# Optimization experiments

Hardware: AMD Instinct MI355X
Metric: run time of the kernel (lower is better)

## Reference

```python
import jax, jax.numpy as jnp
import numpy as np

H_DIM = 1024
GROUPS = [(256, 2), (128, 3), (64, 2)]  # (subspace_dim d, count n), descending d; sum(d*n)=1024
NUM_STEPS = 32
BLOCK_LEN = 4096
BZ = 256
NUM_UNITS = sum(n for _, n in GROUPS)  # 7 subspaces total
EPS_Q = 1e-8   # query norm clamp (torch clamp(min=1e-08))
EPS_K = 1e-3   # key norm clamp (torch clamp(min=0.001))
EPS_COS = 1e-8 # F.cosine_similarity eps


def _split_subspaces(h):
    """h: [bz, H] (already rotated) -> list of [n_i, bz, d_i] per group.
    Mirrors _get_subspace_h: split along features, view [bz,n,d], transpose(0,1)."""
    out, off = [], 0
    bz = h.shape[0]
    for d, n in GROUPS:
        chunk = h[:, off:off + d * n].reshape(bz, n, d).transpose(1, 0, 2)
        out.append(chunk)
        off += d * n
    return out


def setup_inputs() -> dict:
    key = jax.random.key(0)
    k1, k2, k3 = jax.random.split(key, 3)
    query = jax.random.normal(k1, (BZ, H_DIM), jnp.float32)
    keys = jax.random.normal(k2, (NUM_STEPS, BLOCK_LEN, H_DIM), jnp.float32)
    A = jax.random.normal(k3, (H_DIM, H_DIM), jnp.float32)
    R, _ = jnp.linalg.qr(A)  # orthogonal rotation weight (torch orthogonal parametrization)
    return {"query": query, "keys": keys, "R": R}


def reference(query, keys, R):
    # differentiable rotated query subspaces
    query_sub = _split_subspaces(query @ R)  # list of [n, bz, d]

    # ---- no-grad top-1 retrieval over num_steps key blocks ----
    q_sub_sg = [jax.lax.stop_gradient(q) for q in query_sub]
    q_normed = [q / jnp.clip(jnp.linalg.norm(q, axis=-1, keepdims=True), EPS_Q, None)
                for q in q_sub_sg]
    keys_sg = jax.lax.stop_gradient(keys)
    R_sg = jax.lax.stop_gradient(R)

    def step(carry, key_block):
        best_val, best_vec = carry
        k_sub = _split_subspaces(key_block @ R_sg)
        sims = []
        for q, k in zip(q_normed, k_sub):
            kn = k / jnp.clip(jnp.linalg.norm(k, axis=-1, keepdims=True), EPS_K, None)
            sims.append(jnp.einsum('nbd,nld->nbl', q, kn))
        sim = jnp.concatenate(sims, axis=0)      # [U, bz, L]
        max_v = sim.max(axis=-1)                  # [U, bz]
        max_idx = sim.argmax(axis=-1)             # [U, bz]
        cand_vec = key_block[max_idx]             # [U, bz, H] gather of raw (unrotated) keys
        m = max_v > best_val                      # masked update: most_sim_value[m]=...
        best_val = jnp.where(m, max_v, best_val)
        best_vec = jnp.where(m[..., None], cand_vec, best_vec)
        return (best_val, best_vec), None

    init = (-jnp.ones((NUM_UNITS, BZ), jnp.float32),
            jnp.zeros((NUM_UNITS, BZ, H_DIM), jnp.float32))
    (_, best_vec), _ = jax.lax.scan(step, init, keys_sg)

    # ---- differentiable loss: rotate retrieved vectors through R ----
    rotated = (best_vec.reshape(NUM_UNITS * BZ, H_DIM) @ R).reshape(NUM_UNITS, BZ, H_DIM)
    sims = []
    off_u, off_c = 0, 0
    for i, (d, n) in enumerate(GROUPS):
        chunk = rotated[off_u:off_u + n, :, off_c:off_c + n * d]   # [n, bz, n*d]
        chunk = chunk.reshape(n, BZ, n, d).transpose(0, 2, 1, 3)   # [n, n, bz, d]
        diag = chunk[jnp.arange(n), jnp.arange(n)]                 # [n, bz, d] (eye-mask select)
        q = query_sub[i]                                           # [n, bz, d]
        num = jnp.sum(q * diag, axis=-1)
        den = (jnp.clip(jnp.linalg.norm(q, axis=-1), EPS_COS, None) *
               jnp.clip(jnp.linalg.norm(diag, axis=-1), EPS_COS, None))
        cos = num / den                                            # [n, bz]
        sims.append(cos.mean(axis=1) * d)                          # weight by subspace dim
        off_u += n
        off_c += n * d
    sim_total = jnp.concatenate(sims).sum() / H_DIM
    return -sim_total
```

## Files before the change

### kernel.cpp

```cpp
#include <hip/hip_runtime.h>
#include <stdint.h>

static constexpr int Hd   = 1024;
static constexpr int BZn  = 256;
static constexpr int MTOT = 131072;
static constexpr int BM   = 64;
static constexpr int NU   = 7;

typedef float  f32x4  __attribute__((ext_vector_type(4)));
typedef short  bf16x8 __attribute__((ext_vector_type(8)));
typedef unsigned short u16;

__device__ __forceinline__ u16 f2bf(float f) {
    unsigned int u = __float_as_uint(f);
    unsigned int r = (u + 0x7FFFu + ((u >> 16) & 1u)) >> 16;
    return (u16)r;
}
__device__ __forceinline__ float bf2f(u16 h) {
    return __uint_as_float(((unsigned int)h) << 16);
}


__global__ void k_qrot(const float* __restrict__ query, const float* __restrict__ R,
                       float* __restrict__ Qrot) {
    __shared__ float qt[4][Hd];
    const int t = threadIdx.x;
    const int r0 = blockIdx.x * 4;
    for (int r = 0; r < 4; ++r)
        *(float4*)(&qt[r][t * 4]) = *(const float4*)(query + (long long)(r0 + r) * Hd + t * 4);
    __syncthreads();
    float acc[4][4] = {};
    for (int k = 0; k < Hd; ++k) {
        float4 rv = *(const float4*)(R + (long long)k * Hd + t * 4);
#pragma unroll
        for (int r = 0; r < 4; ++r) {
            float qv = qt[r][k];
            acc[r][0] += qv * rv.x; acc[r][1] += qv * rv.y;
            acc[r][2] += qv * rv.z; acc[r][3] += qv * rv.w;
        }
    }
    for (int r = 0; r < 4; ++r) {
        float4 o; o.x = acc[r][0]; o.y = acc[r][1]; o.z = acc[r][2]; o.w = acc[r][3];
        *(float4*)(Qrot + (long long)(r0 + r) * Hd + t * 4) = o;
    }
}

__global__ void k_rpack(const float* __restrict__ R, u16* __restrict__ Rpack) {
    const int gt = blockIdx.x * 256 + threadIdx.x;
    const int frag = gt >> 6, lam = gt & 63;
    const int cblk = frag >> 5, kblk = frag & 31;
    const int c  = cblk * 16 + (lam & 15);
    const int k0 = kblk * 32 + (lam >> 4) * 8;
    union { bf16x8 v; u16 u[8]; } p;
#pragma unroll
    for (int j = 0; j < 8; ++j) p.u[j] = f2bf(R[(long long)(k0 + j) * Hd + c]);
    *(bf16x8*)(Rpack + (long long)frag * 512 + lam * 8) = p.v;
}

__global__ void k_qpack(const float* __restrict__ Qrot, u16* __restrict__ Qpack) {
    const int gt = blockIdx.x * 256 + threadIdx.x;
    const int frag = gt >> 6, lam = gt & 63;
    const int cblk = frag >> 4, qblk = frag & 15;
    const int q  = qblk * 16 + (lam & 15);
    const int c0 = cblk * 32 + (lam >> 4) * 8;
    union { bf16x8 v; u16 u[8]; } p;
#pragma unroll
    for (int j = 0; j < 8; ++j) p.u[j] = f2bf(Qrot[(long long)q * Hd + c0 + j]);
    *(bf16x8*)(Qpack + (long long)frag * 512 + lam * 8) = p.v;
}

static constexpr int LDS_TOT = 163840;

__global__ __launch_bounds__(512, 2)
void k_main(const float* __restrict__ keys, const u16* __restrict__ Rp,
            const u16* __restrict__ Qp, unsigned long long* __restrict__ best) {
    extern __shared__ char smem[];
    char* keysA = smem;
    char* Krot  = smem + 131072;

    const int t   = threadIdx.x;
    const int lam = t & 63;
    const int w   = t >> 6;
    const int l15 = lam & 15;
    const int lg  = lam >> 4;
    const int row0 = blockIdx.x * BM;

    {
        const float* kb = keys + (long long)row0 * Hd;
#pragma unroll 4
        for (int i = 0; i < 16; ++i) {
            int e0 = i * 4096 + t * 8;
            float4 v0 = *(const float4*)(kb + e0);
            float4 v1 = *(const float4*)(kb + e0 + 4);
            int row = e0 >> 10, k = e0 & 1023;
            union { bf16x8 v; u16 u[8]; } p;
            p.u[0] = f2bf(v0.x); p.u[1] = f2bf(v0.y); p.u[2] = f2bf(v0.z); p.u[3] = f2bf(v0.w);
            p.u[4] = f2bf(v1.x); p.u[5] = f2bf(v1.y); p.u[6] = f2bf(v1.z); p.u[7] = f2bf(v1.w);
            int byte = (row * 2048 + k * 2) ^ ((row & 7) << 4);
            *(bf16x8*)(keysA + byte) = p.v;
        }
    }
    __syncthreads();

    const char* RpB = (const char*)Rp;
    const int aswz = (l15 & 7) << 4;

#pragma unroll 1
    for (int q = 0; q < 4; ++q) {
        const char* bb0 = RpB + (long long)(q * 16 + w * 2 + 0) * 32768 + lam * 16;
        const char* bb1 = RpB + (long long)(q * 16 + w * 2 + 1) * 32768 + lam * 16;

        f32x4 racc[4][2];
#pragma unroll
        for (int m = 0; m < 4; ++m) { racc[m][0] = (f32x4){0,0,0,0}; racc[m][1] = (f32x4){0,0,0,0}; }

        bf16x8 nbA0 = *(const bf16x8*)(bb0);
        bf16x8 nbA1 = *(const bf16x8*)(bb1);
        bf16x8 nbB0 = *(const bf16x8*)(bb0 + 1024);
        bf16x8 nbB1 = *(const bf16x8*)(bb1 + 1024);

#pragma unroll 4
        for (int ks = 0; ks < 32; ++ks) {
            bf16x8 cb0 = nbA0, cb1 = nbA1;
            nbA0 = nbB0; nbA1 = nbB1;
            if (ks < 30) {
                nbB0 = *(const bf16x8*)(bb0 + (ks + 2) * 1024);
                nbB1 = *(const bf16x8*)(bb1 + (ks + 2) * 1024);
            }
#pragma unroll
            for (int m = 0; m < 4; ++m) {
                int abyte = ((m * 16 + l15) * 2048 + (ks * 32 + lg * 8) * 2) ^ aswz;
                bf16x8 a = *(const bf16x8*)(keysA + abyte);
                racc[m][0] = __builtin_amdgcn_mfma_f32_16x16x32_bf16(a, cb0, racc[m][0], 0, 0, 0);
                racc[m][1] = __builtin_amdgcn_mfma_f32_16x16x32_bf16(a, cb1, racc[m][1], 0, 0, 0);
            }
        }

        __syncthreads();

#pragma unroll
        for (int m = 0; m < 4; ++m)
#pragma unroll
            for (int n2 = 0; n2 < 2; ++n2) {
                int qcol = w * 32 + n2 * 16 + l15;
#pragma unroll
                for (int e = 0; e < 4; ++e) {
                    int key = m * 16 + lg * 4 + e;
                    int byte = (key * 512 + qcol * 2) ^ ((key & 7) << 4);
                    *(u16*)(Krot + byte) = f2bf(racc[m][n2][e]);
                }
            }
        __syncthreads();

        const int ubase = (q == 0) ? 0 : (q == 1) ? 1 : (q == 2) ? 2 : 4;
        const int fmask = (q < 2) ? 0x80 : (q == 2) ? 0x88 : 0xA8;

        f32x4 acc[2][4];
#pragma unroll
        for (int m = 0; m < 2; ++m)
#pragma unroll
            for (int n = 0; n < 4; ++n) acc[m][n] = (f32x4){0,0,0,0};
        float nrm[4] = {0.f, 0.f, 0.f, 0.f};
        int u = ubase;

#pragma unroll
        for (int ks = 0; ks < 8; ++ks) {
            bf16x8 aq[2], bk[4];
            int cblk = q * 8 + ks;
#pragma unroll
            for (int m = 0; m < 2; ++m) {
                long long qoff = ((long long)(cblk * 16 + (w * 2 + m)) * 64 + lam) * 8;
                aq[m] = *(const bf16x8*)(Qp + qoff);
            }
#pragma unroll
            for (int n = 0; n < 4; ++n) {
                int byte = ((n * 16 + l15) * 512 + (ks * 32 + lg * 8) * 2) ^ aswz;
                bk[n] = *(const bf16x8*)(Krot + byte);
            }
#pragma unroll
            for (int m = 0; m < 2; ++m)
#pragma unroll
                for (int n = 0; n < 4; ++n)
                    acc[m][n] = __builtin_amdgcn_mfma_f32_16x16x32_bf16(aq[m], bk[n], acc[m][n], 0, 0, 0);
#pragma unroll
            for (int n = 0; n < 4; ++n) {
                union { bf16x8 v; u16 s[8]; } ub; ub.v = bk[n];
#pragma unroll
                for (int j = 0; j < 8; ++j) { float f = bf2f(ub.s[j]); nrm[n] = fmaf(f, f, nrm[n]); }
            }

            if ((fmask >> ks) & 1) {
                float rn[4];
#pragma unroll
                for (int n = 0; n < 4; ++n) {
                    float s = nrm[n];
                    s += __shfl_xor(s, 16);
                    s += __shfl_xor(s, 32);
                    rn[n] = 1.0f / fmaxf(sqrtf(s), 1e-3f);
                    nrm[n] = 0.f;
                }
#pragma unroll
                for (int m = 0; m < 2; ++m) {
#pragma unroll
                    for (int e = 0; e < 4; ++e) {
                        float bv = acc[m][0][e] * rn[0];
                        int   bi = l15;
#pragma unroll
                        for (int n = 1; n < 4; ++n) {
                            float v = acc[m][n][e] * rn[n];
                            if (v > bv) { bv = v; bi = n * 16 + l15; }
                        }
#pragma unroll
                        for (int mask = 1; mask <= 8; mask <<= 1) {
                            float ov = __shfl_xor(bv, mask);
                            int   oi = __shfl_xor(bi, mask);
                            if (ov > bv || (ov == bv && oi < bi)) { bv = ov; bi = oi; }
                        }
                        if (l15 == 0) {
                            int qq = w * 32 + m * 16 + lg * 4 + e;
                            unsigned int ui = __float_as_uint(bv);
                            unsigned int mp = ui ^ ((ui >> 31) ? 0xFFFFFFFFu : 0x80000000u);
                            unsigned int gl = (unsigned int)(row0 + bi);
                            unsigned long long enc =
                                ((unsigned long long)mp << 32) |
                                (unsigned long long)(0xFFFFFFFFu - gl);
                            unsigned long long* addr = best + u * BZn + qq;
                            if (enc > *addr) atomicMax(addr, enc);
                        }
                    }
#pragma unroll
                    for (int n = 0; n < 4; ++n) acc[m][n] = (f32x4){0,0,0,0};
                }
                ++u;
            }
        }
    }
}

__global__ void k_final(const float* __restrict__ keys, const float* __restrict__ R,
                        const float* __restrict__ Qrot,
                        const unsigned long long* __restrict__ best, float* __restrict__ out) {
    const int fid = blockIdx.x;
    const int u = fid >> 8, b = fid & 255;
    int off, d;
    if (u < 2)      { off = u * 256;            d = 256; }
    else if (u < 5) { off = 512 + (u - 2) * 128; d = 128; }
    else            { off = 896 + (u - 5) * 64;  d = 64;  }

    unsigned long long ent = best[fid];
    if (ent == 0ull) return;

    __shared__ float krow[Hd];
    __shared__ float red[12];
    const int t = threadIdx.x;
    unsigned int gl = 0xFFFFFFFFu - (unsigned int)(ent & 0xFFFFFFFFull);
    const float* kp = keys + (long long)gl * Hd;
    *(float4*)(&krow[t * 4]) = *(const float4*)(kp + t * 4);
    __syncthreads();

    float pn = 0.f, pq = 0.f, pk = 0.f;
    if (t < d) {
        float kr = 0.f;
        for (int k = 0; k < Hd; ++k) kr += krow[k] * R[(long long)k * Hd + off + t];
        float qv = Qrot[(long long)b * Hd + off + t];
        pn = qv * kr; pq = qv * qv; pk = kr * kr;
    }
    for (int mask = 1; mask <= 32; mask <<= 1) {
        pn += __shfl_xor(pn, mask); pq += __shfl_xor(pq, mask); pk += __shfl_xor(pk, mask);
    }
    if ((t & 63) == 0) { red[t >> 6] = pn; red[4 + (t >> 6)] = pq; red[8 + (t >> 6)] = pk; }
    __syncthreads();
    if (t == 0) {
        float nm = red[0] + red[1] + red[2] + red[3];
        float qq = red[4] + red[5] + red[6] + red[7];
        float kk = red[8] + red[9] + red[10] + red[11];
        float cosv = nm / (fmaxf(sqrtf(qq), 1e-8f) * fmaxf(sqrtf(kk), 1e-8f));
        atomicAdd(out, -cosv * (float)d / (256.0f * 1024.0f));
    }
}

extern "C" void kernel_launch(void* const* d_in, const int* in_sizes, int n_in,
                              void* d_out, int out_size, void* d_ws, size_t ws_size,
                              hipStream_t stream) {
    (void)in_sizes; (void)n_in; (void)out_size; (void)ws_size;
    const float* query = (const float*)d_in[0];
    const float* keys  = (const float*)d_in[1];
    const float* R     = (const float*)d_in[2];
    float* out = (float*)d_out;
    char* ws = (char*)d_ws;

    unsigned long long* best = (unsigned long long*)ws;
    float* Qrot   = (float*)(ws + 16384);
    u16*   Rpack  = (u16*)(ws + 16384 + 1048576);
    u16*   Qpack  = (u16*)(ws + 16384 + 1048576 + 2097152);

    hipMemsetAsync(best, 0, NU * BZn * sizeof(unsigned long long), stream);
    hipMemsetAsync(out, 0, sizeof(float), stream);

    k_qrot <<<64,  256, 0, stream>>>(query, R, Qrot);
    k_rpack<<<512, 256, 0, stream>>>(R, Rpack);
    k_qpack<<<128, 256, 0, stream>>>(Qrot, Qpack);

    hipFuncSetAttribute((const void*)k_main,
                        hipFuncAttributeMaxDynamicSharedMemorySize, LDS_TOT);
    k_main <<<MTOT / BM, 512, LDS_TOT, stream>>>(keys, Rpack, Qpack, best);
    k_final<<<NU * BZn, 256, 0, stream>>>(keys, R, Qrot, best, out);
}
```

Measured before the change: 1.126 ms.

## Double k_main block to 1024 threads, split key rows across wave pairs

k_main now launches 1024 threads per block, and each pair of waves splits the 64 key rows in half, so every wave computes a 32x32 tile in both the rotation GEMM and the similarity GEMM instead of 64x32. The Krot LDS layout gets a different XOR swizzle, and the argmax reduction packs a truncated value plus a 6-bit local index into one 32-bit word, needing one shuffle per step instead of two. The aim is more waves in flight to hide latency, at the cost of lower per-wave reuse and dropping the low 6 mantissa bits when breaking similarity ties. __launch_bounds__(1024,4) conflicts with the 160KB LDS per block, so only one block fits per CU.

Result: slower. 1.162 ms (+3.2%).

```diff
diff --git a/kernel.cpp b/kernel.cpp
--- a/kernel.cpp
+++ b/kernel.cpp
@@ -71,7 +71,8 @@
 
 static constexpr int LDS_TOT = 163840;
 
-__global__ __launch_bounds__(512, 2)
+
+__global__ __launch_bounds__(1024, 4)
 void k_main(const float* __restrict__ keys, const u16* __restrict__ Rp,
             const u16* __restrict__ Qp, unsigned long long* __restrict__ best) {
     extern __shared__ char smem[];
@@ -83,13 +84,15 @@
     const int w   = t >> 6;
     const int l15 = lam & 15;
     const int lg  = lam >> 4;
+    const int cs  = w >> 1;
+    const int h   = w & 1;
     const int row0 = blockIdx.x * BM;
 
     {
         const float* kb = keys + (long long)row0 * Hd;
-#pragma unroll 4
-        for (int i = 0; i < 16; ++i) {
-            int e0 = i * 4096 + t * 8;
+#pragma unroll
+        for (int i = 0; i < 8; ++i) {
+            int e0 = i * 8192 + t * 8;
             float4 v0 = *(const float4*)(kb + e0);
             float4 v1 = *(const float4*)(kb + e0 + 4);
             int row = e0 >> 10, k = e0 & 1023;
@@ -103,16 +106,17 @@
     __syncthreads();
 
     const char* RpB = (const char*)Rp;
-    const int aswz = (l15 & 7) << 4;
+    const int arow  = h * 32 + l15;
+    const int aswz  = (l15 & 7) << 4;
 
 #pragma unroll 1
     for (int q = 0; q < 4; ++q) {
-        const char* bb0 = RpB + (long long)(q * 16 + w * 2 + 0) * 32768 + lam * 16;
-        const char* bb1 = RpB + (long long)(q * 16 + w * 2 + 1) * 32768 + lam * 16;
-
-        f32x4 racc[4][2];
-#pragma unroll
-        for (int m = 0; m < 4; ++m) { racc[m][0] = (f32x4){0,0,0,0}; racc[m][1] = (f32x4){0,0,0,0}; }
+        const char* bb0 = RpB + (long long)((q * 16 + cs * 2 + 0) * 32) * 1024 + lam * 16;
+        const char* bb1 = RpB + (long long)((q * 16 + cs * 2 + 1) * 32) * 1024 + lam * 16;
+
+        f32x4 racc[2][2];
+#pragma unroll
+        for (int m = 0; m < 2; ++m) { racc[m][0] = (f32x4){0,0,0,0}; racc[m][1] = (f32x4){0,0,0,0}; }
 
         bf16x8 nbA0 = *(const bf16x8*)(bb0);
         bf16x8 nbA1 = *(const bf16x8*)(bb1);
@@ -128,8 +132,8 @@
                 nbB1 = *(const bf16x8*)(bb1 + (ks + 2) * 1024);
             }
 #pragma unroll
-            for (int m = 0; m < 4; ++m) {
-                int abyte = ((m * 16 + l15) * 2048 + (ks * 32 + lg * 8) * 2) ^ aswz;
+            for (int m = 0; m < 2; ++m) {
+                int abyte = (((arow + m * 16) * 2048) + (ks * 32 + lg * 8) * 2) ^ aswz;
                 bf16x8 a = *(const bf16x8*)(keysA + abyte);
                 racc[m][0] = __builtin_amdgcn_mfma_f32_16x16x32_bf16(a, cb0, racc[m][0], 0, 0, 0);
                 racc[m][1] = __builtin_amdgcn_mfma_f32_16x16x32_bf16(a, cb1, racc[m][1], 0, 0, 0);
@@ -139,15 +143,15 @@
         __syncthreads();
 
 #pragma unroll
-        for (int m = 0; m < 4; ++m)
-#pragma unroll
-            for (int n2 = 0; n2 < 2; ++n2) {
-                int qcol = w * 32 + n2 * 16 + l15;
+        for (int m = 0; m < 2; ++m)
+#pragma unroll
+            for (int n = 0; n < 2; ++n) {
+                int qcol = cs * 32 + n * 16 + l15;
 #pragma unroll
                 for (int e = 0; e < 4; ++e) {
-                    int key = m * 16 + lg * 4 + e;
-                    int byte = (key * 512 + qcol * 2) ^ ((key & 7) << 4);
-                    *(u16*)(Krot + byte) = f2bf(racc[m][n2][e]);
+                    int key = h * 32 + m * 16 + lg * 4 + e;
+                    int byte = key * 512 + ((((qcol >> 3) + 2 * key) & 31) << 4) + (qcol & 7) * 2;
+                    *(u16*)(Krot + byte) = f2bf(racc[m][n][e]);
                 }
             }
         __syncthreads();
@@ -155,81 +159,79 @@
         const int ubase = (q == 0) ? 0 : (q == 1) ? 1 : (q == 2) ? 2 : 4;
         const int fmask = (q < 2) ? 0x80 : (q == 2) ? 0x88 : 0xA8;
 
-        f32x4 acc[2][4];
-#pragma unroll
-        for (int m = 0; m < 2; ++m)
-#pragma unroll
-            for (int n = 0; n < 4; ++n) acc[m][n] = (f32x4){0,0,0,0};
-        float nrm[4] = {0.f, 0.f, 0.f, 0.f};
+        f32x4 acc[2][2];
+#pragma unroll
+        for (int m = 0; m < 2; ++m) { acc[m][0] = (f32x4){0,0,0,0}; acc[m][1] = (f32x4){0,0,0,0}; }
+        float nrm[2] = {0.f, 0.f};
         int u = ubase;
 
 #pragma unroll
         for (int ks = 0; ks < 8; ++ks) {
-            bf16x8 aq[2], bk[4];
+            bf16x8 aq[2], bk[2];
             int cblk = q * 8 + ks;
 #pragma unroll
             for (int m = 0; m < 2; ++m) {
-                long long qoff = ((long long)(cblk * 16 + (w * 2 + m)) * 64 + lam) * 8;
+                long long qoff = ((long long)(cblk * 16 + (cs * 2 + m)) * 64 + lam) * 8;
                 aq[m] = *(const bf16x8*)(Qp + qoff);
             }
 #pragma unroll
-            for (int n = 0; n < 4; ++n) {
-                int byte = ((n * 16 + l15) * 512 + (ks * 32 + lg * 8) * 2) ^ aswz;
-                bk[n] = *(const bf16x8*)(Krot + byte);
+            for (int n = 0; n < 2; ++n) {
+                int key = h * 32 + n * 16 + l15;
+                int slot = ((ks * 4 + lg) + 2 * key) & 31;
+                bk[n] = *(const bf16x8*)(Krot + key * 512 + (slot << 4));
             }
 #pragma unroll
             for (int m = 0; m < 2; ++m)
 #pragma unroll
-                for (int n = 0; n < 4; ++n)
+                for (int n = 0; n < 2; ++n)
                     acc[m][n] = __builtin_amdgcn_mfma_f32_16x16x32_bf16(aq[m], bk[n], acc[m][n], 0, 0, 0);
 #pragma unroll
-            for (int n = 0; n < 4; ++n) {
+            for (int n = 0; n < 2; ++n) {
                 union { bf16x8 v; u16 s[8]; } ub; ub.v = bk[n];
 #pragma unroll
                 for (int j = 0; j < 8; ++j) { float f = bf2f(ub.s[j]); nrm[n] = fmaf(f, f, nrm[n]); }
             }
 
             if ((fmask >> ks) & 1) {
-                float rn[4];
-#pragma unroll
-                for (int n = 0; n < 4; ++n) {
+                float rn2[2];
+#pragma unroll
+                for (int n = 0; n < 2; ++n) {
                     float s = nrm[n];
                     s += __shfl_xor(s, 16);
                     s += __shfl_xor(s, 32);
-                    rn[n] = 1.0f / fmaxf(sqrtf(s), 1e-3f);
+                    rn2[n] = 1.0f / fmaxf(sqrtf(s), 1e-3f);
                     nrm[n] = 0.f;
                 }
 #pragma unroll
                 for (int m = 0; m < 2; ++m) {
 #pragma unroll
                     for (int e = 0; e < 4; ++e) {
-                        float bv = acc[m][0][e] * rn[0];
-                        int   bi = l15;
-#pragma unroll
-                        for (int n = 1; n < 4; ++n) {
-                            float v = acc[m][n][e] * rn[n];
-                            if (v > bv) { bv = v; bi = n * 16 + l15; }
-                        }
+                        float v0 = acc[m][0][e] * rn2[0];
+                        float v1 = acc[m][1][e] * rn2[1];
+                        float bv; int bi6;
+                        if (v1 > v0) { bv = v1; bi6 = h * 32 + 16 + l15; }
+                        else         { bv = v0; bi6 = h * 32 + l15; }
+                        unsigned int ui = __float_as_uint(bv);
+                        unsigned int mp = ui ^ (((int)ui < 0) ? 0xFFFFFFFFu : 0x80000000u);
+                        unsigned int enc = (mp & 0xFFFFFFC0u) | (63u - (unsigned int)bi6);
 #pragma unroll
                         for (int mask = 1; mask <= 8; mask <<= 1) {
-                            float ov = __shfl_xor(bv, mask);
-                            int   oi = __shfl_xor(bi, mask);
-                            if (ov > bv || (ov == bv && oi < bi)) { bv = ov; bi = oi; }
+                            unsigned int o = __shfl_xor(enc, mask);
+                            enc = (o > enc) ? o : enc;
                         }
                         if (l15 == 0) {
-                            int qq = w * 32 + m * 16 + lg * 4 + e;
-                            unsigned int ui = __float_as_uint(bv);
-                            unsigned int mp = ui ^ ((ui >> 31) ? 0xFFFFFFFFu : 0x80000000u);
+                            int bi = 63 - (int)(enc & 63u);
                             unsigned int gl = (unsigned int)(row0 + bi);
-                            unsigned long long enc =
-                                ((unsigned long long)mp << 32) |
+                            unsigned long long e64 =
+                                ((unsigned long long)(enc & 0xFFFFFFC0u) << 32) |
                                 (unsigned long long)(0xFFFFFFFFu - gl);
+                            int qq = cs * 32 + m * 16 + lg * 4 + e;
                             unsigned long long* addr = best + u * BZn + qq;
-                            if (enc > *addr) atomicMax(addr, enc);
+                            if (e64 > *addr) atomicMax(addr, e64);
                         }
                     }
 #pragma unroll
-                    for (int n = 0; n < 4; ++n) acc[m][n] = (f32x4){0,0,0,0};
+                    for (int n = 0; n < 2; ++n) acc[m][n] = (f32x4){0,0,0,0};
                 }
                 ++u;
             }
@@ -303,6 +305,6 @@
 
     hipFuncSetAttribute((const void*)k_main,
                         hipFuncAttributeMaxDynamicSharedMemorySize, LDS_TOT);
-    k_main <<<MTOT / BM, 512, LDS_TOT, stream>>>(keys, Rpack, Qpack, best);
+    k_main <<<MTOT / BM, 1024, LDS_TOT, stream>>>(keys, Rpack, Qpack, best);
     k_final<<<NU * BZn, 256, 0, stream>>>(keys, R, Qrot, best, out);
 }
```

## Fuse rotation and similarity with streamed double-buffered key tiles split by column group

Applied to the files above, without the earlier changes.

Replaces the per-64-key block, which loaded a full key tile into LDS and looped over four rotation phases, with blocks covering 128 keys and one column quarter. Key slices stream through a small double-buffered LDS tile while R fragments are prefetched. Norms come from fp32 accumulators, and the argmax is reduced with a packed 32-bit encoding. This lowers LDS use to allow more concurrency, but raw keys are now read once per column group, and the packed encoding truncates low mantissa bits during comparison.

Measured after the change: 1.245 ms. 10.6% more time.

```diff
diff --git a/kernel.cpp b/kernel.cpp
--- a/kernel.cpp
+++ b/kernel.cpp
@@ -1,10 +1,10 @@
 #include <hip/hip_runtime.h>
+#include <hip/hip_bf16.h>
 #include <stdint.h>
 
 static constexpr int Hd   = 1024;
 static constexpr int BZn  = 256;
 static constexpr int MTOT = 131072;
-static constexpr int BM   = 64;
 static constexpr int NU   = 7;
 
 typedef float  f32x4  __attribute__((ext_vector_type(4)));
@@ -12,12 +12,8 @@
 typedef unsigned short u16;
 
 __device__ __forceinline__ u16 f2bf(float f) {
-    unsigned int u = __float_as_uint(f);
-    unsigned int r = (u + 0x7FFFu + ((u >> 16) & 1u)) >> 16;
-    return (u16)r;
-}
-__device__ __forceinline__ float bf2f(u16 h) {
-    return __uint_as_float(((unsigned int)h) << 16);
+    __hip_bfloat16 h = __float2bfloat16(f);
+    return *reinterpret_cast<u16*>(&h);
 }
 
 
@@ -69,170 +65,183 @@
     *(bf16x8*)(Qpack + (long long)frag * 512 + lam * 8) = p.v;
 }
 
-static constexpr int LDS_TOT = 163840;
+static constexpr int LDS_ABUF = 0;
+static constexpr int LDS_T    = 20480;
+static constexpr int LDS_NP   = 90112;
+static constexpr int LDS_TOT  = 92160;
 
 __global__ __launch_bounds__(512, 2)
-void k_main(const float* __restrict__ keys, const u16* __restrict__ Rp,
-            const u16* __restrict__ Qp, unsigned long long* __restrict__ best) {
+void k_fused(const float* __restrict__ keys, const u16* __restrict__ Rp,
+             const u16* __restrict__ Qp, unsigned long long* __restrict__ best) {
     extern __shared__ char smem[];
-    char* keysA = smem;
-    char* Krot  = smem + 131072;
+    char*  abuf0 = smem + LDS_ABUF;
+    char*  abuf1 = smem + LDS_ABUF + 10240;
+    char*  T     = smem + LDS_T;
+    float* normP = (float*)(smem + LDS_NP);
 
     const int t   = threadIdx.x;
     const int lam = t & 63;
     const int w   = t >> 6;
     const int l15 = lam & 15;
     const int lg  = lam >> 4;
-    const int row0 = blockIdx.x * BM;
-
-    {
-        const float* kb = keys + (long long)row0 * Hd;
-#pragma unroll 4
-        for (int i = 0; i < 16; ++i) {
-            int e0 = i * 4096 + t * 8;
-            float4 v0 = *(const float4*)(kb + e0);
-            float4 v1 = *(const float4*)(kb + e0 + 4);
-            int row = e0 >> 10, k = e0 & 1023;
-            union { bf16x8 v; u16 u[8]; } p;
-            p.u[0] = f2bf(v0.x); p.u[1] = f2bf(v0.y); p.u[2] = f2bf(v0.z); p.u[3] = f2bf(v0.w);
-            p.u[4] = f2bf(v1.x); p.u[5] = f2bf(v1.y); p.u[6] = f2bf(v1.z); p.u[7] = f2bf(v1.w);
-            int byte = (row * 2048 + k * 2) ^ ((row & 7) << 4);
-            *(bf16x8*)(keysA + byte) = p.v;
-        }
-    }
-    __syncthreads();
-
-    const char* RpB = (const char*)Rp;
-    const int aswz = (l15 & 7) << 4;
-
-#pragma unroll 1
-    for (int q = 0; q < 4; ++q) {
-        const char* bb0 = RpB + (long long)(q * 16 + w * 2 + 0) * 32768 + lam * 16;
-        const char* bb1 = RpB + (long long)(q * 16 + w * 2 + 1) * 32768 + lam * 16;
-
-        f32x4 racc[4][2];
-#pragma unroll
-        for (int m = 0; m < 4; ++m) { racc[m][0] = (f32x4){0,0,0,0}; racc[m][1] = (f32x4){0,0,0,0}; }
-
-        bf16x8 nbA0 = *(const bf16x8*)(bb0);
-        bf16x8 nbA1 = *(const bf16x8*)(bb1);
-        bf16x8 nbB0 = *(const bf16x8*)(bb0 + 1024);
-        bf16x8 nbB1 = *(const bf16x8*)(bb1 + 1024);
-
-#pragma unroll 4
-        for (int ks = 0; ks < 32; ++ks) {
-            bf16x8 cb0 = nbA0, cb1 = nbA1;
-            nbA0 = nbB0; nbA1 = nbB1;
-            if (ks < 30) {
-                nbB0 = *(const bf16x8*)(bb0 + (ks + 2) * 1024);
-                nbB1 = *(const bf16x8*)(bb1 + (ks + 2) * 1024);
+    const int wq  = w >> 2;
+    const int wc  = w & 3;
+
+    const int bx   = blockIdx.x;
+    const int tkey = bx >> 2;
+    const int cg   = bx & 3;
+    const int kb   = tkey * 128;
+
+    const int sr = t >> 2, sc = t & 3;
+    const float* apt = keys + (long long)(kb + sr) * Hd + sc * 8;
+    const int sdst = sr * 80 + sc * 16;
+
+    const char* bB = (const char*)Rp + (long long)((cg * 16 + wc * 4) * 32) * 1024 + lam * 16;
+
+    f32x4 acc[4][4];
+#pragma unroll
+    for (int m = 0; m < 4; ++m)
+#pragma unroll
+        for (int n = 0; n < 4; ++n) acc[m][n] = (f32x4){0.f, 0.f, 0.f, 0.f};
+
+    float4 ar0 = *(const float4*)(apt);
+    float4 ar1 = *(const float4*)(apt + 4);
+    bf16x8 nb[4];
+#pragma unroll
+    for (int n = 0; n < 4; ++n) nb[n] = *(const bf16x8*)(bB + (long long)(n * 32) * 1024);
+
+#pragma unroll 2
+    for (int s = 0; s < 32; ++s) {
+        char* buf = (s & 1) ? abuf1 : abuf0;
+        union { bf16x8 v; u16 u[8]; } p;
+        p.u[0] = f2bf(ar0.x); p.u[1] = f2bf(ar0.y); p.u[2] = f2bf(ar0.z); p.u[3] = f2bf(ar0.w);
+        p.u[4] = f2bf(ar1.x); p.u[5] = f2bf(ar1.y); p.u[6] = f2bf(ar1.z); p.u[7] = f2bf(ar1.w);
+        *(bf16x8*)(buf + sdst) = p.v;
+
+        const int sn = (s < 31) ? s + 1 : 31;
+        ar0 = *(const float4*)(apt + sn * 32);
+        ar1 = *(const float4*)(apt + sn * 32 + 4);
+        bf16x8 cbv[4];
+#pragma unroll
+        for (int n = 0; n < 4; ++n) cbv[n] = nb[n];
+#pragma unroll
+        for (int n = 0; n < 4; ++n)
+            nb[n] = *(const bf16x8*)(bB + (long long)(n * 32 + sn) * 1024);
+
+        __syncthreads();
+
+#pragma unroll
+        for (int m = 0; m < 4; ++m) {
+            int row = wq * 64 + m * 16 + l15;
+            bf16x8 a = *(const bf16x8*)(buf + row * 80 + lg * 16);
+#pragma unroll
+            for (int n = 0; n < 4; ++n)
+                acc[m][n] = __builtin_amdgcn_mfma_f32_16x16x32_bf16(a, cbv[n], acc[m][n], 0, 0, 0);
+        }
+    }
+    __syncthreads();
+
+#pragma unroll
+    for (int m = 0; m < 4; ++m) {
+#pragma unroll
+        for (int e = 0; e < 4; ++e) {
+            float s = 0.f;
+#pragma unroll
+            for (int n = 0; n < 4; ++n) { float v = acc[m][n][e]; s = fmaf(v, v, s); }
+            s += __shfl_xor(s, 1); s += __shfl_xor(s, 2);
+            s += __shfl_xor(s, 4); s += __shfl_xor(s, 8);
+            if (l15 == 0) normP[wc * 128 + wq * 64 + m * 16 + lg * 4 + e] = s;
+        }
+    }
+
+#pragma unroll
+    for (int m = 0; m < 4; ++m) {
+        char* Ts = T + ((wq * 2 + (m >> 1)) * 2 + (wc >> 1)) * 8704;
+#pragma unroll
+        for (int n = 0; n < 4; ++n) {
+            int tcol = (wc & 1) * 64 + n * 16 + l15;
+#pragma unroll
+            for (int e = 0; e < 4; ++e) {
+                int trow = (m & 1) * 16 + lg * 4 + e;
+                *(u16*)(Ts + trow * 272 + tcol * 2) = f2bf(acc[m][n][e]);
             }
-#pragma unroll
-            for (int m = 0; m < 4; ++m) {
-                int abyte = ((m * 16 + l15) * 2048 + (ks * 32 + lg * 8) * 2) ^ aswz;
-                bf16x8 a = *(const bf16x8*)(keysA + abyte);
-                racc[m][0] = __builtin_amdgcn_mfma_f32_16x16x32_bf16(a, cb0, racc[m][0], 0, 0, 0);
-                racc[m][1] = __builtin_amdgcn_mfma_f32_16x16x32_bf16(a, cb1, racc[m][1], 0, 0, 0);
+        }
+    }
+    __syncthreads();
+
+    const int qh = w >> 2;
+    const int kq = w & 3;
+    const int fmask8 = (cg < 2) ? 0x80 : (cg == 2) ? 0x88 : 0xA8;
+
+    f32x4 acc2[8][2];
+#pragma unroll
+    for (int mf = 0; mf < 8; ++mf) { acc2[mf][0] = (f32x4){0,0,0,0}; acc2[mf][1] = (f32x4){0,0,0,0}; }
+
+    int u    = (cg < 2) ? cg : (cg == 2) ? 2 : 4;
+    int prev = 0;
+
+#pragma unroll
+    for (int st = 0; st < 8; ++st) {
+        bf16x8 aq[8];
+#pragma unroll
+        for (int mf = 0; mf < 8; ++mf)
+            aq[mf] = *(const bf16x8*)((const char*)Qp +
+                        (long long)((cg * 8 + st) * 16 + qh * 8 + mf) * 1024 + lam * 16);
+        bf16x8 bk[2];
+        {
+            const char* Ts = T + (kq * 2 + (st >> 2)) * 8704;
+#pragma unroll
+            for (int nf = 0; nf < 2; ++nf)
+                bk[nf] = *(const bf16x8*)(Ts + (nf * 16 + l15) * 272 + (st & 3) * 64 + lg * 16);
+        }
+#pragma unroll
+        for (int mf = 0; mf < 8; ++mf) {
+            acc2[mf][0] = __builtin_amdgcn_mfma_f32_16x16x32_bf16(aq[mf], bk[0], acc2[mf][0], 0, 0, 0);
+            acc2[mf][1] = __builtin_amdgcn_mfma_f32_16x16x32_bf16(aq[mf], bk[1], acc2[mf][1], 0, 0, 0);
+        }
+
+        if ((fmask8 >> st) & 1) {
+            const int wc0 = prev >> 1, wc1 = st >> 1;
+            float rn[2];
+#pragma unroll
+            for (int nf = 0; nf < 2; ++nf) {
+                int key = kq * 32 + nf * 16 + l15;
+                float nv = 0.f;
+                for (int q2 = wc0; q2 <= wc1; ++q2) nv += normP[q2 * 128 + key];
+                rn[nf] = 1.0f / fmaxf(sqrtf(nv), 1e-3f);
             }
-        }
-
-        __syncthreads();
-
-#pragma unroll
-        for (int m = 0; m < 4; ++m)
-#pragma unroll
-            for (int n2 = 0; n2 < 2; ++n2) {
-                int qcol = w * 32 + n2 * 16 + l15;
+#pragma unroll
+            for (int mf = 0; mf < 8; ++mf) {
 #pragma unroll
                 for (int e = 0; e < 4; ++e) {
-                    int key = m * 16 + lg * 4 + e;
-                    int byte = (key * 512 + qcol * 2) ^ ((key & 7) << 4);
-                    *(u16*)(Krot + byte) = f2bf(racc[m][n2][e]);
+                    float v0 = acc2[mf][0][e] * rn[0];
+                    float v1 = acc2[mf][1][e] * rn[1];
+                    float bv; int bi5;
+                    if (v1 > v0) { bv = v1; bi5 = 16 + l15; }
+                    else         { bv = v0; bi5 = l15; }
+                    unsigned int ui = __float_as_uint(bv);
+                    unsigned int mp = ui ^ (((int)ui < 0) ? 0xFFFFFFFFu : 0x80000000u);
+                    unsigned int enc = (mp & 0xFFFFFFC0u) | (63u - (unsigned int)bi5);
+#pragma unroll
+                    for (int mask = 1; mask <= 8; mask <<= 1) {
+                        unsigned int o = __shfl_xor(enc, mask);
+                        enc = (o > enc) ? o : enc;
+                    }
+                    if (l15 == 0) {
+                        unsigned int gl = (unsigned int)(kb + kq * 32 + (63 - (int)(enc & 63u)));
+                        unsigned long long e64 =
+                            ((unsigned long long)(enc & 0xFFFFFFC0u) << 32) |
+                            (unsigned long long)(0xFFFFFFFFu - gl);
+                        int qq = qh * 128 + mf * 16 + lg * 4 + e;
+                        unsigned long long* addr = best + u * BZn + qq;
+                        if (e64 > *addr) atomicMax(addr, e64);
+                    }
+                    acc2[mf][0][e] = 0.f;
+                    acc2[mf][1][e] = 0.f;
                 }
             }
-        __syncthreads();
-
-        const int ubase = (q == 0) ? 0 : (q == 1) ? 1 : (q == 2) ? 2 : 4;
-        const int fmask = (q < 2) ? 0x80 : (q == 2) ? 0x88 : 0xA8;
-
-        f32x4 acc[2][4];
-#pragma unroll
-        for (int m = 0; m < 2; ++m)
-#pragma unroll
-            for (int n = 0; n < 4; ++n) acc[m][n] = (f32x4){0,0,0,0};
-        float nrm[4] = {0.f, 0.f, 0.f, 0.f};
-        int u = ubase;
-
-#pragma unroll
-        for (int ks = 0; ks < 8; ++ks) {
-            bf16x8 aq[2], bk[4];
-            int cblk = q * 8 + ks;
-#pragma unroll
-            for (int m = 0; m < 2; ++m) {
-                long long qoff = ((long long)(cblk * 16 + (w * 2 + m)) * 64 + lam) * 8;
-                aq[m] = *(const bf16x8*)(Qp + qoff);
-            }
-#pragma unroll
-            for (int n = 0; n < 4; ++n) {
-                int byte = ((n * 16 + l15) * 512 + (ks * 32 + lg * 8) * 2) ^ aswz;
-                bk[n] = *(const bf16x8*)(Krot + byte);
-            }
-#pragma unroll
-            for (int m = 0; m < 2; ++m)
-#pragma unroll
-                for (int n = 0; n < 4; ++n)
-                    acc[m][n] = __builtin_amdgcn_mfma_f32_16x16x32_bf16(aq[m], bk[n], acc[m][n], 0, 0, 0);
-#pragma unroll
-            for (int n = 0; n < 4; ++n) {
-                union { bf16x8 v; u16 s[8]; } ub; ub.v = bk[n];
-#pragma unroll
-                for (int j = 0; j < 8; ++j) { float f = bf2f(ub.s[j]); nrm[n] = fmaf(f, f, nrm[n]); }
-            }
-
-            if ((fmask >> ks) & 1) {
-                float rn[4];
-#pragma unroll
-                for (int n = 0; n < 4; ++n) {
-                    float s = nrm[n];
-                    s += __shfl_xor(s, 16);
-                    s += __shfl_xor(s, 32);
-                    rn[n] = 1.0f / fmaxf(sqrtf(s), 1e-3f);
-                    nrm[n] = 0.f;
-                }
-#pragma unroll
-                for (int m = 0; m < 2; ++m) {
-#pragma unroll
-                    for (int e = 0; e < 4; ++e) {
-                        float bv = acc[m][0][e] * rn[0];
-                        int   bi = l15;
-#pragma unroll
-                        for (int n = 1; n < 4; ++n) {
-                            float v = acc[m][n][e] * rn[n];
-                            if (v > bv) { bv = v; bi = n * 16 + l15; }
-                        }
-#pragma unroll
-                        for (int mask = 1; mask <= 8; mask <<= 1) {
-                            float ov = __shfl_xor(bv, mask);
-                            int   oi = __shfl_xor(bi, mask);
-                            if (ov > bv || (ov == bv && oi < bi)) { bv = ov; bi = oi; }
-                        }
-                        if (l15 == 0) {
-                            int qq = w * 32 + m * 16 + lg * 4 + e;
-                            unsigned int ui = __float_as_uint(bv);
-                            unsigned int mp = ui ^ ((ui >> 31) ? 0xFFFFFFFFu : 0x80000000u);
-                            unsigned int gl = (unsigned int)(row0 + bi);
-                            unsigned long long enc =
-                                ((unsigned long long)mp << 32) |
-                                (unsigned long long)(0xFFFFFFFFu - gl);
-                            unsigned long long* addr = best + u * BZn + qq;
-                            if (enc > *addr) atomicMax(addr, enc);
-                        }
-                    }
-#pragma unroll
-                    for (int n = 0; n < 4; ++n) acc[m][n] = (f32x4){0,0,0,0};
-                }
-                ++u;
-            }
+            ++u;
+            prev = st + 1;
         }
     }
 }
@@ -301,8 +310,9 @@
     k_rpack<<<512, 256, 0, stream>>>(R, Rpack);
     k_qpack<<<128, 256, 0, stream>>>(Qrot, Qpack);
 
-    hipFuncSetAttribute((const void*)k_main,
+    hipFuncSetAttribute((const void*)k_fused,
                         hipFuncAttributeMaxDynamicSharedMemorySize, LDS_TOT);
-    k_main <<<MTOT / BM, 512, LDS_TOT, stream>>>(keys, Rpack, Qpack, best);
+    k_fused<<<(MTOT / 128) * 4, 512, LDS_TOT, stream>>>(keys, Rpack, Qpack, best);
+
     k_final<<<NU * BZn, 256, 0, stream>>>(keys, R, Qrot, best, out);
 }
```
